# Performance work log

Measured on AMD Instinct MI355X. Metric: run time of the kernel, lower is better.

Reference implementation:

```python
import jax, jax.numpy as jnp
import numpy as np

N_CROPS = 64
K = 128          # keypoints per crop (uniform ragged special case)
D = 128          # descriptor dim
KNN = 20
NQ = 20
MIN_V, MAX_V = 0.0, 1.0


def setup_inputs() -> dict:
    key = jax.random.key(0)
    k1, k2 = jax.random.split(key)
    b = N_CROPS * K
    anc = jax.random.normal(k1, (b, D), dtype=jnp.float32)
    pos = jax.random.normal(k2, (b, D), dtype=jnp.float32)
    # L2-normalized descriptors so similarities fall in the quantizer range
    anc = anc / jnp.linalg.norm(anc, axis=1, keepdims=True)
    pos = pos / jnp.linalg.norm(pos, axis=1, keepdims=True)
    kpts_crop_ids = np.full((N_CROPS,), K, dtype=np.int32)
    return {"anc_feat": anc, "pos_feat": pos, "kpts_crop_ids": kpts_crop_ids}


def _neg_cols(n_crops, k, b):
    # Static per-crop column indices into sim_neg_all (width b-1), excluding
    # the same-crop negative block [i*k, i*k + (k-1)) exactly as the torch code.
    all_c = np.arange(b - 1)
    cols = []
    for i in range(n_crops):
        c = i * k
        cols.append(np.concatenate([all_c[:c], all_c[c + k - 1:]]))
    return np.stack(cols)  # [n_crops, b-k]


def compute_ap(x, label, nq=NQ, min_v=MIN_V, max_v=MAX_V):
    # R2D2 APLoss.compute_AP: fixed 1x1-conv quantizer -> triangular bins
    a = (nq - 1) / (max_v - min_v)
    w1 = np.full(nq, -a, np.float32)
    b1 = (a * min_v + np.arange(nq, 0, -1)).astype(np.float32)
    w2 = np.full(nq, a, np.float32)
    b2 = (np.arange(2 - nq, 2) - a * min_v).astype(np.float32)
    w1[0], b1[0] = 0.0, 1.0     # first line of 1st half: horizontal
    w2[-1], b2[-1] = 0.0, 1.0   # last line of 2nd half: horizontal
    xq = x[:, None, :]
    q = jnp.minimum(w1[None, :, None] * xq + b1[None, :, None],
                    w2[None, :, None] * xq + b2[None, :, None])
    q = jnp.clip(q, 0.0)                                 # N x Q x M
    nbs = q.sum(-1)                                      # N x Q
    rec = (q * label[:, None, :]).sum(-1)                # N x Q
    prec = jnp.cumsum(rec, -1) / (1e-16 + jnp.cumsum(nbs, -1))
    rec = rec / rec.sum(-1, keepdims=True)
    return (prec * rec).sum(-1)                          # per-query AP, [N]


def reference(anc_feat, pos_feat, kpts_crop_ids):
    ks = np.asarray(kpts_crop_ids)
    assert np.all(ks == ks[0]) and int(ks[0]) > 1, "uniform crops, >1 kpt each"
    k = int(ks[0]); n_crops = ks.shape[0]; b = n_crops * k
    sim = anc_feat @ pos_feat.T                          # [b, b]
    sim_pos = jnp.diagonal(sim)[:, None]                 # [b, 1]
    # drop diagonal -> [b, b-1] (row-major off-diagonal, same as mtx[~eye])
    sim_neg_all = sim.reshape(-1)[:-1].reshape(b - 1, b + 1)[:, 1:].reshape(b, b - 1)
    cols = jnp.asarray(_neg_cols(n_crops, k, b))         # [n_crops, b-k]
    blocks = sim_neg_all.reshape(n_crops, k, b - 1)
    # exclude same-crop negatives per crop (static gather), then hard-neg top-k
    excl = jnp.take_along_axis(blocks, cols[:, None, :], axis=2)  # [n_crops, k, b-k]
    top, _ = jax.lax.top_k(excl, KNN)                    # sorted descending == sort[:, :knn]
    sim_neg = top.reshape(b, KNN)
    sim_final = jnp.concatenate([sim_pos, sim_neg], axis=1)      # [b, knn+1]
    lbl_final = jnp.zeros_like(sim_final).at[:, 0].set(1.0)
    ap = compute_ap(sim_final, lbl_final)
    return (1.0 - ap).mean(), ap.mean()
```

## Files before the change

### kernel.cpp

```cpp
#include <hip/hip_runtime.h>

#define B_TOT 8192
#define DIM 128
#define KNN 20
#define NQ 20

#define RPB 128
#define SLICE 1024
#define NSLICE 8
#define NSTEP 16
#define CBUF 128
#define FLAG_AT 63

typedef float f32x4 __attribute__((ext_vector_type(4)));
typedef short short8 __attribute__((ext_vector_type(8)));

__device__ __forceinline__ unsigned short f2bf(float f) {
  unsigned u = __float_as_uint(f);
  return (unsigned short)((u + 0x7FFFu + ((u >> 16) & 1u)) >> 16);
}
__device__ __forceinline__ float bf2f(unsigned short u) {
  return __uint_as_float(((unsigned)u) << 16);
}

__global__ __launch_bounds__(256) void cvt_bf16(
    const float* __restrict__ a, const float* __restrict__ p,
    unsigned short* __restrict__ ab, unsigned short* __restrict__ pb) {
  const int i = (blockIdx.x * 256 + threadIdx.x) * 4;
  const float4 va = *reinterpret_cast<const float4*>(a + i);
  const float4 vp = *reinterpret_cast<const float4*>(p + i);
  ushort4 ra, rp;
  ra.x = f2bf(va.x); ra.y = f2bf(va.y); ra.z = f2bf(va.z); ra.w = f2bf(va.w);
  rp.x = f2bf(vp.x); rp.y = f2bf(vp.y); rp.z = f2bf(vp.z); rp.w = f2bf(vp.w);
  *reinterpret_cast<ushort4*>(ab + i) = ra;
  *reinterpret_cast<ushort4*>(pb + i) = rp;
}

__global__ __launch_bounds__(512, 4) void apk_slice(
    const unsigned short* __restrict__ ancb,
    const unsigned short* __restrict__ posb,
    unsigned short* __restrict__ gTop,
    float* __restrict__ gDiag)
{
  __shared__ unsigned short sBuf[RPB][CBUF];
  __shared__ float sMrg[RPB][4][KNN + 1];
  __shared__ int sCnt[RPB];
  __shared__ float sThr[RPB];
  __shared__ int sFlag;

  const int tid = threadIdx.x;
  const int wave = tid >> 6;
  const int lane = tid & 63;
  const int rt = wave >> 1;
  const int cg = wave & 1;
  const int l15 = lane & 15;
  const int g = lane >> 4;
  const int rg = blockIdx.x >> 3;
  const int cs = blockIdx.x & 7;
  const int rBase = rg * RPB;
  const int sx0 = (cs == (rg >> 3)) ? (rg & 7) * 2 : -9;

  for (int i = tid; i < RPB; i += 512) { sCnt[i] = 0; sThr[i] = -1e30f; }
  if (tid == 0) sFlag = 0;
  __syncthreads();

  short8 afr[2][4];
#pragma unroll
  for (int rsub = 0; rsub < 2; ++rsub) {
    const short8* arow = reinterpret_cast<const short8*>(
        ancb + (size_t)(rBase + rt * 32 + rsub * 16 + l15) * DIM);
#pragma unroll
    for (int kk = 0; kk < 4; ++kk) afr[rsub][kk] = arow[kk * 4 + g];
  }

  float thrv[2][4];
#pragma unroll
  for (int rsub = 0; rsub < 2; ++rsub)
#pragma unroll
    for (int q = 0; q < 4; ++q) thrv[rsub][q] = -1e30f;

  for (int s = 0; s < NSTEP; ++s) {
    const int c0 = cs * SLICE + s * 64 + cg * 32 + l15;
    short8 bfr[2][4];
#pragma unroll
    for (int csub = 0; csub < 2; ++csub) {
      const unsigned short* bp = posb + (size_t)(c0 + csub * 16) * DIM + g * 8;
#pragma unroll
      for (int kk = 0; kk < 4; ++kk)
        bfr[csub][kk] = *reinterpret_cast<const short8*>(bp + kk * 32);
    }
    f32x4 acc[2][2];
#pragma unroll
    for (int rsub = 0; rsub < 2; ++rsub)
#pragma unroll
      for (int csub = 0; csub < 2; ++csub) {
        acc[rsub][csub] = 0.f;
#pragma unroll
        for (int kk = 0; kk < 4; ++kk)
          acc[rsub][csub] = __builtin_amdgcn_mfma_f32_16x16x32_bf16(
              afr[rsub][kk], bfr[csub][kk], acc[rsub][csub], 0, 0, 0);
      }

    if (s == sx0 || s == sx0 + 1) {
      const int soff = s - sx0;
#pragma unroll
      for (int rsub = 0; rsub < 2; ++rsub)
#pragma unroll
        for (int csub = 0; csub < 2; ++csub)
#pragma unroll
          for (int q = 0; q < 4; ++q) {
            const int row_l = rt * 32 + rsub * 16 + g * 4 + q;
            const int col_l = cg * 32 + csub * 16 + l15;
            if (row_l == soff * 64 + col_l)
              gDiag[rBase + row_l] = acc[rsub][csub][q];
          }
    } else {
#pragma unroll
      for (int rsub = 0; rsub < 2; ++rsub)
#pragma unroll
        for (int q = 0; q < 4; ++q) {
          const int row_l = rt * 32 + rsub * 16 + g * 4 + q;
          const float thr = thrv[rsub][q];
          const float v0 = acc[rsub][0][q];
          const float v1 = acc[rsub][1][q];
          if (fmaxf(v0, v1) > thr) {
            if (v0 > thr) {
              const int idx = atomicAdd(&sCnt[row_l], 1);
              if (idx >= FLAG_AT) sFlag = 1;
              if (idx < CBUF) sBuf[row_l][idx] = f2bf(v0);
            }
            if (v1 > thr) {
              const int idx = atomicAdd(&sCnt[row_l], 1);
              if (idx >= FLAG_AT) sFlag = 1;
              if (idx < CBUF) sBuf[row_l][idx] = f2bf(v1);
            }
          }
        }
    }

    __syncthreads();
    const int flag = sFlag;
    __syncthreads();

    if (flag != 0 || s == NSTEP - 1) {
      const int row = tid >> 2;
      const int h = tid & 3;
      const int cnt = min(sCnt[row], CBUF);
      float tk[KNN];
#pragma unroll
      for (int q = 0; q < KNN; ++q) tk[q] = -1e30f;
      for (int i = 0; i < CBUF / 4; ++i) {
        const int idx = h + i * 4;
        if (idx < cnt) {
          const float v = bf2f(sBuf[row][idx]);
          if (v > tk[0]) {
            float x = v;
#pragma unroll
            for (int p = 0; p < KNN - 1; ++p) {
              const float nxt = tk[p + 1];
              tk[p] = fminf(x, nxt);
              x = fmaxf(x, nxt);
            }
            tk[KNN - 1] = x;
          }
        }
      }
#pragma unroll
      for (int q = 0; q < KNN; ++q) sMrg[row][h][q] = tk[q];
      if (h < 2) {
        float out[KNN];
        int a = KNN - 1, b = KNN - 1;
#pragma unroll
        for (int o = KNN - 1; o >= 0; --o) {
          const float va = (a >= 0) ? sMrg[row][h][a] : -3e30f;
          const float vb = (b >= 0) ? sMrg[row][h + 2][b] : -3e30f;
          if (va >= vb) { out[o] = va; --a; } else { out[o] = vb; --b; }
        }
#pragma unroll
        for (int q = 0; q < KNN; ++q) sMrg[row][h][q] = out[q];
      }
      if (h == 0) {
        float out[KNN];
        int a = KNN - 1, b = KNN - 1;
#pragma unroll
        for (int o = KNN - 1; o >= 0; --o) {
          const float va = (a >= 0) ? sMrg[row][0][a] : -3e30f;
          const float vb = (b >= 0) ? sMrg[row][1][b] : -3e30f;
          if (va >= vb) { out[o] = va; --a; } else { out[o] = vb; --b; }
        }
        if (cnt > KNN) {
          sThr[row] = out[0];
#pragma unroll
          for (int q = 0; q < KNN; ++q) sBuf[row][q] = f2bf(out[q]);
          sCnt[row] = KNN;
        }
      }
      if (tid == 0) sFlag = 0;
      __syncthreads();
#pragma unroll
      for (int rsub = 0; rsub < 2; ++rsub)
#pragma unroll
        for (int q = 0; q < 4; ++q)
          thrv[rsub][q] = sThr[rt * 32 + rsub * 16 + g * 4 + q];
    }
  }

  for (int i = tid; i < RPB * KNN; i += 512) {
    const int row = i / KNN, j = i % KNN;
    const unsigned short v =
        (j < sCnt[row]) ? sBuf[row][j] : f2bf(-1e30f);
    gTop[(size_t)(rBase + row) * (NSLICE * KNN) + cs * KNN + j] = v;
  }
}

__global__ __launch_bounds__(256) void apk_reduce(
    const unsigned short* __restrict__ gTop, const float* __restrict__ gDiag,
    float* __restrict__ apsum)
{
  const int row = blockIdx.x * 256 + threadIdx.x;
  float tk[KNN];
#pragma unroll
  for (int q = 0; q < KNN; ++q) tk[q] = -1e30f;
  const unsigned short* tp = gTop + (size_t)row * (NSLICE * KNN);
  for (int i = 0; i < NSLICE * KNN; ++i) {
    const float v = bf2f(tp[i]);
    if (v > tk[0]) {
      float x = v;
#pragma unroll
      for (int p = 0; p < KNN - 1; ++p) {
        const float nxt = tk[p + 1];
        tk[p] = fminf(x, nxt);
        x = fmaxf(x, nxt);
      }
      tk[KNN - 1] = x;
    }
  }
  float x[KNN + 1];
  x[0] = gDiag[row];
#pragma unroll
  for (int q = 0; q < KNN; ++q) x[q + 1] = tk[q];
  float cum_rec = 0.f, cum_nbs = 0.f, ap_num = 0.f;
#pragma unroll 1
  for (int qi = 0; qi < NQ; ++qi) {
    const float w1 = (qi == 0) ? 0.f : -19.f;
    const float c1 = (qi == 0) ? 1.f : (float)(20 - qi);
    const float w2 = (qi == NQ - 1) ? 0.f : 19.f;
    const float c2 = (qi == NQ - 1) ? 1.f : (float)(qi - 18);
    float nbs = 0.f, rec = 0.f;
#pragma unroll
    for (int jx = 0; jx < KNN + 1; ++jx) {
      const float xv = x[jx];
      float qv = fminf(fmaf(w1, xv, c1), fmaf(w2, xv, c2));
      qv = fmaxf(qv, 0.f);
      nbs += qv;
      if (jx == 0) rec = qv;
    }
    cum_rec += rec;
    cum_nbs += nbs;
    ap_num = fmaf(cum_rec / (1e-16f + cum_nbs), rec, ap_num);
  }
  float ap = ap_num / cum_rec;
#pragma unroll
  for (int o = 1; o < 64; o <<= 1) ap += __shfl_xor(ap, o, 64);
  if ((threadIdx.x & 63) == 0) atomicAdd(apsum, ap);
}

#define F_TM 16
#define F_TN 256
#define F_NTILE (B_TOT / F_TN)
#define F_TPR (F_TN / F_TM)
#define F_SSTRIDE 264
#define KCROP 128

__global__ __launch_bounds__(256) void apk_topk_f32(
    const float* __restrict__ anc, const float* __restrict__ pos,
    float* __restrict__ apsum)
{
  __shared__ __align__(16) float sAnc[F_TM][DIM];
  __shared__ float sSim[F_TM * F_SSTRIDE];
  __shared__ float sTop[F_TM][F_TPR][KNN];
  __shared__ float sDiag[F_TM];
  __shared__ float sAp[F_TM];
  const int tid = threadIdx.x;
  const int rowBase = blockIdx.x * F_TM;
  for (int idx = tid; idx < F_TM * DIM; idx += 256)
    sAnc[idx / DIM][idx % DIM] = anc[rowBase * DIM + idx];
  __syncthreads();
  float tk[KNN];
#pragma unroll
  for (int q = 0; q < KNN; ++q) tk[q] = -1e30f;
  const int cropLo = (rowBase >> 7) << 7;
  const int myRow = tid / F_TPR;
  const int myLane = tid % F_TPR;
  for (int t = 0; t < F_NTILE; ++t) {
    const int j = t * F_TN + tid;
    float acc[F_TM];
#pragma unroll
    for (int r = 0; r < F_TM; ++r) acc[r] = 0.f;
    const float4* pj = reinterpret_cast<const float4*>(pos + (size_t)j * DIM);
#pragma unroll 2
    for (int k4 = 0; k4 < DIM / 4; ++k4) {
      const float4 p = pj[k4];
#pragma unroll
      for (int r = 0; r < F_TM; ++r) {
        const float4 a = *reinterpret_cast<const float4*>(&sAnc[r][k4 * 4]);
        acc[r] = fmaf(p.x, a.x, acc[r]);
        acc[r] = fmaf(p.y, a.y, acc[r]);
        acc[r] = fmaf(p.z, a.z, acc[r]);
        acc[r] = fmaf(p.w, a.w, acc[r]);
      }
    }
    if (j >= rowBase && j < rowBase + F_TM) sDiag[j - rowBase] = acc[j - rowBase];
    __syncthreads();
#pragma unroll
    for (int r = 0; r < F_TM; ++r) sSim[r * F_SSTRIDE + tid] = acc[r];
    __syncthreads();
    const int jbase = t * F_TN;
#pragma unroll
    for (int q = 0; q < F_TN / F_TPR; ++q) {
      const int jj = q * F_TPR + myLane;
      const int jg = jbase + jj;
      const float v = sSim[myRow * F_SSTRIDE + jj];
      if ((unsigned)(jg - cropLo) >= (unsigned)KCROP && v > tk[0]) {
        float x = v;
#pragma unroll
        for (int p = 0; p < KNN - 1; ++p) {
          const float nxt = tk[p + 1];
          tk[p] = fminf(x, nxt);
          x = fmaxf(x, nxt);
        }
        tk[KNN - 1] = x;
      }
    }
  }
  __syncthreads();
#pragma unroll
  for (int q = 0; q < KNN; ++q) sTop[myRow][myLane][q] = tk[q];
  __syncthreads();
  for (int step = F_TPR / 2; step > 0; step >>= 1) {
    if (myLane < step) {
      float out[KNN];
      int a = KNN - 1, b = KNN - 1;
#pragma unroll
      for (int o = KNN - 1; o >= 0; --o) {
        const float va = (a >= 0) ? sTop[myRow][myLane][a] : -3e30f;
        const float vb = (b >= 0) ? sTop[myRow][myLane + step][b] : -3e30f;
        if (va >= vb) { out[o] = va; --a; } else { out[o] = vb; --b; }
      }
#pragma unroll
      for (int q = 0; q < KNN; ++q) sTop[myRow][myLane][q] = out[q];
    }
    __syncthreads();
  }
  if (tid < F_TM) {
    float x[KNN + 1];
    x[0] = sDiag[tid];
#pragma unroll
    for (int q = 0; q < KNN; ++q) x[q + 1] = sTop[tid][0][q];
    float cum_rec = 0.f, cum_nbs = 0.f, ap_num = 0.f;
#pragma unroll 1
    for (int qi = 0; qi < NQ; ++qi) {
      const float w1 = (qi == 0) ? 0.f : -19.f;
      const float c1 = (qi == 0) ? 1.f : (float)(20 - qi);
      const float w2 = (qi == NQ - 1) ? 0.f : 19.f;
      const float c2 = (qi == NQ - 1) ? 1.f : (float)(qi - 18);
      float nbs = 0.f, rec = 0.f;
#pragma unroll
      for (int jx = 0; jx < KNN + 1; ++jx) {
        const float xv = x[jx];
        float qv = fminf(fmaf(w1, xv, c1), fmaf(w2, xv, c2));
        qv = fmaxf(qv, 0.f);
        nbs += qv;
        if (jx == 0) rec = qv;
      }
      cum_rec += rec;
      cum_nbs += nbs;
      ap_num = fmaf(cum_rec / (1e-16f + cum_nbs), rec, ap_num);
    }
    sAp[tid] = ap_num / cum_rec;
  }
  __syncthreads();
  if (tid == 0) {
    float s = 0.f;
#pragma unroll
    for (int r = 0; r < F_TM; ++r) s += sAp[r];
    atomicAdd(apsum, s);
  }
}

__global__ void apk_final(const float* __restrict__ apsum, float* __restrict__ out) {
  const float m = *apsum * (1.f / (float)B_TOT);
  out[0] = 1.f - m;
  out[1] = m;
}

extern "C" void kernel_launch(void* const* d_in, const int* in_sizes, int n_in,
                              void* d_out, int out_size, void* d_ws, size_t ws_size,
                              hipStream_t stream) {
  const float* anc = (const float*)d_in[0];
  const float* pos = (const float*)d_in[1];
  const size_t bf_bytes = (size_t)B_TOT * DIM * sizeof(unsigned short);
  const size_t top_bytes = (size_t)B_TOT * NSLICE * KNN * sizeof(unsigned short);
  const size_t diag_bytes = (size_t)B_TOT * sizeof(float);
  const size_t off_top = 2 * bf_bytes;
  const size_t off_diag = off_top + ((top_bytes + 15) & ~(size_t)15);
  const size_t off_sum = off_diag + ((diag_bytes + 15) & ~(size_t)15);
  const size_t need = off_sum + 16;
  if (ws_size >= need) {
    unsigned short* ancb = (unsigned short*)d_ws;
    unsigned short* posb = ancb + (size_t)B_TOT * DIM;
    unsigned short* gTop = (unsigned short*)((char*)d_ws + off_top);
    float* gDiag = (float*)((char*)d_ws + off_diag);
    float* apsum = (float*)((char*)d_ws + off_sum);
    hipMemsetAsync(apsum, 0, sizeof(float), stream);
    cvt_bf16<<<(B_TOT * DIM) / (256 * 4), 256, 0, stream>>>(anc, pos, ancb, posb);
    apk_slice<<<64 * NSLICE, 512, 0, stream>>>(ancb, posb, gTop, gDiag);
    apk_reduce<<<B_TOT / 256, 256, 0, stream>>>(gTop, gDiag, apsum);
    apk_final<<<1, 1, 0, stream>>>(apsum, (float*)d_out);
  } else {
    float* apsum = (float*)d_ws;
    hipMemsetAsync(apsum, 0, sizeof(float), stream);
    apk_topk_f32<<<B_TOT / F_TM, 256, 0, stream>>>(anc, pos, apsum);
    apk_final<<<1, 1, 0, stream>>>(apsum, (float*)d_out);
  }
}
```

Before: 247.5 us.

## Replace threshold-buffer top-k with two-pass histogram radix select

The per-slice top-k selection is restructured into two passes. The first pass builds a 64-bin per-row histogram of similarities with shared atomics and derives a per-row threshold bin. The second pass recomputes the MFMA tile and buffers only candidates at or above that bin, followed by a single final top-k merge. This removes the repeated flag checks, double barriers and mid-loop merges, but it doubles the MFMA and B-load work. It also risks silently dropping candidates when more than 64 values fall in the threshold bin, and it stores merge values in bf16.

```diff
diff --git a/kernel.cpp b/kernel.cpp
--- a/kernel.cpp
+++ b/kernel.cpp
@@ -9,8 +9,9 @@
 #define SLICE 1024
 #define NSLICE 8
 #define NSTEP 16
-#define CBUF 128
-#define FLAG_AT 63
+#define NBIN 64
+#define CBUF 64
+#define CSTRIDE 66
 
 typedef float f32x4 __attribute__((ext_vector_type(4)));
 typedef short short8 __attribute__((ext_vector_type(8)));
@@ -21,6 +22,10 @@
 }
 __device__ __forceinline__ float bf2f(unsigned short u) {
   return __uint_as_float(((unsigned)u) << 16);
+}
+__device__ __forceinline__ int binof(float v) {
+  int b = (int)((v + 1.0f) * 32.0f);
+  return min(NBIN - 1, max(0, b));
 }
 
 __global__ __launch_bounds__(256) void cvt_bf16(
@@ -36,17 +41,16 @@
   *reinterpret_cast<ushort4*>(pb + i) = rp;
 }
 
-__global__ __launch_bounds__(512, 4) void apk_slice(
+__global__ __launch_bounds__(512) void apk_slice(
     const unsigned short* __restrict__ ancb,
     const unsigned short* __restrict__ posb,
     unsigned short* __restrict__ gTop,
     float* __restrict__ gDiag)
 {
-  __shared__ unsigned short sBuf[RPB][CBUF];
-  __shared__ float sMrg[RPB][4][KNN + 1];
+  __shared__ unsigned int sHist[RPB][NBIN];
+  __shared__ unsigned short sBuf[RPB][CSTRIDE];
   __shared__ int sCnt[RPB];
-  __shared__ float sThr[RPB];
-  __shared__ int sFlag;
+  __shared__ int sThrB[RPB];
 
   const int tid = threadIdx.x;
   const int wave = tid >> 6;
@@ -60,9 +64,8 @@
   const int rBase = rg * RPB;
   const int sx0 = (cs == (rg >> 3)) ? (rg & 7) * 2 : -9;
 
-  for (int i = tid; i < RPB; i += 512) { sCnt[i] = 0; sThr[i] = -1e30f; }
-  if (tid == 0) sFlag = 0;
-  __syncthreads();
+  for (int i = tid; i < RPB * NBIN; i += 512) (&sHist[0][0])[i] = 0u;
+  for (int i = tid; i < RPB; i += 512) sCnt[i] = 0;
 
   short8 afr[2][4];
 #pragma unroll
@@ -72,35 +75,28 @@
 #pragma unroll
     for (int kk = 0; kk < 4; ++kk) afr[rsub][kk] = arow[kk * 4 + g];
   }
-
-  float thrv[2][4];
-#pragma unroll
-  for (int rsub = 0; rsub < 2; ++rsub)
-#pragma unroll
-    for (int q = 0; q < 4; ++q) thrv[rsub][q] = -1e30f;
-
+  __syncthreads();
+
+#define LOADB_MFMA(S)                                                         \
+  const int c0 = cs * SLICE + (S) * 64 + cg * 32 + l15;                       \
+  short8 bfr[2][4];                                                           \
+  _Pragma("unroll") for (int csub = 0; csub < 2; ++csub) {                    \
+    const unsigned short* bp = posb + (size_t)(c0 + csub * 16) * DIM + g * 8; \
+    _Pragma("unroll") for (int kk = 0; kk < 4; ++kk)                          \
+      bfr[csub][kk] = *reinterpret_cast<const short8*>(bp + kk * 32);         \
+  }                                                                           \
+  f32x4 acc[2][2];                                                            \
+  _Pragma("unroll") for (int rsub = 0; rsub < 2; ++rsub)                      \
+  _Pragma("unroll") for (int csub = 0; csub < 2; ++csub) {                    \
+    acc[rsub][csub] = 0.f;                                                    \
+    _Pragma("unroll") for (int kk = 0; kk < 4; ++kk)                          \
+      acc[rsub][csub] = __builtin_amdgcn_mfma_f32_16x16x32_bf16(              \
+          afr[rsub][kk], bfr[csub][kk], acc[rsub][csub], 0, 0, 0);            \
+  }
+
+#pragma unroll 2
   for (int s = 0; s < NSTEP; ++s) {
-    const int c0 = cs * SLICE + s * 64 + cg * 32 + l15;
-    short8 bfr[2][4];
-#pragma unroll
-    for (int csub = 0; csub < 2; ++csub) {
-      const unsigned short* bp = posb + (size_t)(c0 + csub * 16) * DIM + g * 8;
-#pragma unroll
-      for (int kk = 0; kk < 4; ++kk)
-        bfr[csub][kk] = *reinterpret_cast<const short8*>(bp + kk * 32);
-    }
-    f32x4 acc[2][2];
-#pragma unroll
-    for (int rsub = 0; rsub < 2; ++rsub)
-#pragma unroll
-      for (int csub = 0; csub < 2; ++csub) {
-        acc[rsub][csub] = 0.f;
-#pragma unroll
-        for (int kk = 0; kk < 4; ++kk)
-          acc[rsub][csub] = __builtin_amdgcn_mfma_f32_16x16x32_bf16(
-              afr[rsub][kk], bfr[csub][kk], acc[rsub][csub], 0, 0, 0);
-      }
-
+    LOADB_MFMA(s)
     if (s == sx0 || s == sx0 + 1) {
       const int soff = s - sx0;
 #pragma unroll
@@ -120,96 +116,99 @@
 #pragma unroll
         for (int q = 0; q < 4; ++q) {
           const int row_l = rt * 32 + rsub * 16 + g * 4 + q;
-          const float thr = thrv[rsub][q];
-          const float v0 = acc[rsub][0][q];
-          const float v1 = acc[rsub][1][q];
-          if (fmaxf(v0, v1) > thr) {
-            if (v0 > thr) {
-              const int idx = atomicAdd(&sCnt[row_l], 1);
-              if (idx >= FLAG_AT) sFlag = 1;
-              if (idx < CBUF) sBuf[row_l][idx] = f2bf(v0);
-            }
-            if (v1 > thr) {
-              const int idx = atomicAdd(&sCnt[row_l], 1);
-              if (idx >= FLAG_AT) sFlag = 1;
-              if (idx < CBUF) sBuf[row_l][idx] = f2bf(v1);
-            }
-          }
+          atomicAdd(&sHist[row_l][binof(acc[rsub][0][q])], 1u);
+          atomicAdd(&sHist[row_l][binof(acc[rsub][1][q])], 1u);
         }
     }
-
-    __syncthreads();
-    const int flag = sFlag;
-    __syncthreads();
-
-    if (flag != 0 || s == NSTEP - 1) {
-      const int row = tid >> 2;
-      const int h = tid & 3;
-      const int cnt = min(sCnt[row], CBUF);
-      float tk[KNN];
-#pragma unroll
-      for (int q = 0; q < KNN; ++q) tk[q] = -1e30f;
-      for (int i = 0; i < CBUF / 4; ++i) {
-        const int idx = h + i * 4;
-        if (idx < cnt) {
-          const float v = bf2f(sBuf[row][idx]);
-          if (v > tk[0]) {
-            float x = v;
-#pragma unroll
-            for (int p = 0; p < KNN - 1; ++p) {
-              const float nxt = tk[p + 1];
-              tk[p] = fminf(x, nxt);
-              x = fmaxf(x, nxt);
-            }
-            tk[KNN - 1] = x;
-          }
+  }
+  __syncthreads();
+
+  if (tid < RPB) {
+    int cum = 0, bstar = 0;
+    for (int b = NBIN - 1; b >= 0; --b) {
+      cum += (int)sHist[tid][b];
+      if (cum >= KNN) { bstar = b; break; }
+    }
+    sThrB[tid] = bstar;
+  }
+  __syncthreads();
+
+  int thrb[2][4];
+#pragma unroll
+  for (int rsub = 0; rsub < 2; ++rsub)
+#pragma unroll
+    for (int q = 0; q < 4; ++q)
+      thrb[rsub][q] = sThrB[rt * 32 + rsub * 16 + g * 4 + q];
+
+#pragma unroll 2
+  for (int s = 0; s < NSTEP; ++s) {
+    if (s == sx0 || s == sx0 + 1) continue;
+    LOADB_MFMA(s)
+#pragma unroll
+    for (int rsub = 0; rsub < 2; ++rsub)
+#pragma unroll
+      for (int q = 0; q < 4; ++q) {
+        const int row_l = rt * 32 + rsub * 16 + g * 4 + q;
+        const float v0 = acc[rsub][0][q];
+        const float v1 = acc[rsub][1][q];
+        if (binof(v0) >= thrb[rsub][q]) {
+          const int idx = atomicAdd(&sCnt[row_l], 1);
+          if (idx < CBUF) sBuf[row_l][idx] = f2bf(v0);
         }
-      }
-#pragma unroll
-      for (int q = 0; q < KNN; ++q) sMrg[row][h][q] = tk[q];
-      if (h < 2) {
-        float out[KNN];
-        int a = KNN - 1, b = KNN - 1;
-#pragma unroll
-        for (int o = KNN - 1; o >= 0; --o) {
-          const float va = (a >= 0) ? sMrg[row][h][a] : -3e30f;
-          const float vb = (b >= 0) ? sMrg[row][h + 2][b] : -3e30f;
-          if (va >= vb) { out[o] = va; --a; } else { out[o] = vb; --b; }
+        if (binof(v1) >= thrb[rsub][q]) {
+          const int idx = atomicAdd(&sCnt[row_l], 1);
+          if (idx < CBUF) sBuf[row_l][idx] = f2bf(v1);
         }
-#pragma unroll
-        for (int q = 0; q < KNN; ++q) sMrg[row][h][q] = out[q];
-      }
-      if (h == 0) {
-        float out[KNN];
-        int a = KNN - 1, b = KNN - 1;
-#pragma unroll
-        for (int o = KNN - 1; o >= 0; --o) {
-          const float va = (a >= 0) ? sMrg[row][0][a] : -3e30f;
-          const float vb = (b >= 0) ? sMrg[row][1][b] : -3e30f;
-          if (va >= vb) { out[o] = va; --a; } else { out[o] = vb; --b; }
-        }
-        if (cnt > KNN) {
-          sThr[row] = out[0];
-#pragma unroll
-          for (int q = 0; q < KNN; ++q) sBuf[row][q] = f2bf(out[q]);
-          sCnt[row] = KNN;
-        }
-      }
-      if (tid == 0) sFlag = 0;
-      __syncthreads();
-#pragma unroll
-      for (int rsub = 0; rsub < 2; ++rsub)
-#pragma unroll
-        for (int q = 0; q < 4; ++q)
-          thrv[rsub][q] = sThr[rt * 32 + rsub * 16 + g * 4 + q];
-    }
-  }
-
-  for (int i = tid; i < RPB * KNN; i += 512) {
-    const int row = i / KNN, j = i % KNN;
-    const unsigned short v =
-        (j < sCnt[row]) ? sBuf[row][j] : f2bf(-1e30f);
-    gTop[(size_t)(rBase + row) * (NSLICE * KNN) + cs * KNN + j] = v;
+      }
+  }
+  __syncthreads();
+
+  const int row = tid >> 2;
+  const int h = tid & 3;
+  const int cnt = min(sCnt[row], CBUF);
+  float tk[KNN];
+#pragma unroll
+  for (int q = 0; q < KNN; ++q) tk[q] = -1e30f;
+  for (int i = h; i < cnt; i += 4) {
+    const float v = bf2f(sBuf[row][i]);
+    if (v > tk[0]) {
+      float x = v;
+#pragma unroll
+      for (int p = 0; p < KNN - 1; ++p) {
+        const float nxt = tk[p + 1];
+        tk[p] = fminf(x, nxt);
+        x = fmaxf(x, nxt);
+      }
+      tk[KNN - 1] = x;
+    }
+  }
+  unsigned short* mrg = reinterpret_cast<unsigned short*>(&sHist[row][0]);
+#pragma unroll
+  for (int q = 0; q < KNN; ++q) mrg[h * KNN + q] = f2bf(tk[q]);
+  if (h < 2) {
+    float out[KNN];
+    int a = KNN - 1, b = KNN - 1;
+#pragma unroll
+    for (int o = KNN - 1; o >= 0; --o) {
+      const float va = (a >= 0) ? bf2f(mrg[h * KNN + a]) : -3e30f;
+      const float vb = (b >= 0) ? bf2f(mrg[(h + 2) * KNN + b]) : -3e30f;
+      if (va >= vb) { out[o] = va; --a; } else { out[o] = vb; --b; }
+    }
+#pragma unroll
+    for (int q = 0; q < KNN; ++q) mrg[h * KNN + q] = f2bf(out[q]);
+  }
+  if (h == 0) {
+    float out[KNN];
+    int a = KNN - 1, b = KNN - 1;
+#pragma unroll
+    for (int o = KNN - 1; o >= 0; --o) {
+      const float va = (a >= 0) ? bf2f(mrg[a]) : -3e30f;
+      const float vb = (b >= 0) ? bf2f(mrg[KNN + b]) : -3e30f;
+      if (va >= vb) { out[o] = va; --a; } else { out[o] = vb; --b; }
+    }
+#pragma unroll
+    for (int q = 0; q < KNN; ++q)
+      gTop[(size_t)(rBase + row) * (NSLICE * KNN) + cs * KNN + q] = f2bf(out[q]);
   }
 }
 
```

Measured after the change: 246.5 us. Within noise of the previous version (-0.4%).
